# Optimization experiments

Hardware: AMD Instinct MI355X
Metric: run time of the kernel (lower is better)

## Reference

```python
import jax, jax.numpy as jnp
import numpy as np

D_MODEL = 1024
N_EXPERTS = 8
TOP_K = 2


def setup_inputs() -> dict:
    key = jax.random.key(0)
    k1, k2, k3, k4 = jax.random.split(key, 4)
    B, S, D, E = 4, 2048, D_MODEL, N_EXPERTS
    dff = 4 * D
    # xavier-uniform style scale for expert weights
    lim = float(np.sqrt(6.0 / (D + dff)))
    return {
        "x": jax.random.normal(k1, (B, S, D), dtype=jnp.float32),
        "router_w": jax.random.normal(k2, (D, E), dtype=jnp.float32) * (1.0 / np.sqrt(D)),
        "router_b": jnp.zeros((E,), dtype=jnp.float32),
        "expert_up": jax.random.uniform(k3, (E, dff, D), dtype=jnp.float32, minval=-lim, maxval=lim),
        "expert_down": jax.random.uniform(k4, (E, D, dff), dtype=jnp.float32, minval=-lim, maxval=lim),
    }


def reference(x, router_w, router_b, expert_up, expert_down):
    B, S, D = x.shape
    E = expert_up.shape[0]
    x_flat = x.reshape(-1, D)                       # [T, D]
    logits = x_flat @ router_w + router_b           # [T, E]
    probs = jax.nn.softmax(logits, axis=-1)
    top_w, top_idx = jax.lax.top_k(probs, TOP_K)    # [T, K]
    # combine per-token top-k weights into a dense [T, E] combine matrix
    comb = jnp.sum(top_w[..., None] * jax.nn.one_hot(top_idx, E, dtype=x.dtype), axis=1)  # [T, E]
    output = jnp.zeros_like(x_flat)
    for e in range(E):  # fixed small expert count
        h = jax.nn.gelu(x_flat @ expert_up[e].T, approximate=False)   # [T, dff]
        out_e = h @ expert_down[e].T                                  # [T, D]
        output = output + comb[:, e:e + 1] * out_e
    return output.reshape(B, S, D)
```

## Files before the change

kernel.cpp:

```cpp
#include <hip/hip_runtime.h>
#include <hip/hip_bf16.h>
#include <cstdint>

#define T_TOK 8192
#define DM 1024
#define NE 8
#define DFF 4096

#define PERX_UP 576
#define PERX_DN 288
#define GEMM_UP_BLOCKS (8 * PERX_UP)

#define CVTX_BLOCKS 4096
#define CVTW_BLOCKS 16384
#define ROUT_BLOCKS 128

typedef __attribute__((ext_vector_type(8))) short bf16x8;
typedef __attribute__((ext_vector_type(4))) float f32x4;

__device__ __forceinline__ unsigned short f2bf(float f) {
  unsigned int b = __float_as_uint(f);
  b += 0x7FFFu + ((b >> 16) & 1u);
  return (unsigned short)(b >> 16);
}

__device__ __forceinline__ float gelu_exact(float v) {
  return 0.5f * v * (1.0f + erff(v * 0.70710678118654752440f));
}

__device__ __forceinline__ void cvt8(const float* __restrict__ src, unsigned short* __restrict__ dst,
                                     size_t i) {
  const f32x4* p = (const f32x4*)src;
  f32x4 a = p[2 * i];
  f32x4 b = p[2 * i + 1];
  union { bf16x8 v; unsigned short u[8]; } o;
  o.u[0] = f2bf(a.x); o.u[1] = f2bf(a.y); o.u[2] = f2bf(a.z); o.u[3] = f2bf(a.w);
  o.u[4] = f2bf(b.x); o.u[5] = f2bf(b.y); o.u[6] = f2bf(b.z); o.u[7] = f2bf(b.w);
  ((bf16x8*)dst)[i] = o.v;
}

__global__ void cvt_kernel(const float* __restrict__ x, unsigned short* __restrict__ xb) {
  cvt8(x, xb, (size_t)blockIdx.x * blockDim.x + threadIdx.x);
}

__global__ void fused_pre_kernel(const float* __restrict__ x, unsigned short* __restrict__ xb,
                                 const float* __restrict__ up, unsigned short* __restrict__ upb,
                                 const float* __restrict__ rw, const float* __restrict__ rb,
                                 int* __restrict__ counts_pad, int* __restrict__ tlist,
                                 float* __restrict__ wlist) {
  const int bid = blockIdx.x;
  if (bid < CVTX_BLOCKS) {
    cvt8(x, xb, (size_t)bid * 256 + threadIdx.x);
    return;
  }
  if (bid < CVTX_BLOCKS + CVTW_BLOCKS) {
    cvt8(up, upb, (size_t)(bid - CVTX_BLOCKS) * 256 + threadIdx.x);
    return;
  }
  const int rblk = bid - CVTX_BLOCKS - CVTW_BLOCKS;
  __shared__ int hcnt[NE], hbase[NE];
  __shared__ int tE1[64], tE2[64], tR1[64], tR2[64];
  __shared__ float tW1[64], tW2[64];
  if (threadIdx.x < NE) hcnt[threadIdx.x] = 0;
  __syncthreads();
  const int wv = threadIdx.x >> 6, lane = threadIdx.x & 63;
#pragma unroll 1
  for (int it = 0; it < 16; ++it) {
    const int lt = wv * 16 + it;
    const int t = rblk * 64 + lt;
    const float* xr = x + (size_t)t * DM;
    float acc[NE];
#pragma unroll
    for (int e = 0; e < NE; ++e) acc[e] = 0.0f;
#pragma unroll
    for (int i = 0; i < 16; ++i) {
      int d = lane + i * 64;
      float xv = xr[d];
      const float* wr = rw + (size_t)d * NE;
#pragma unroll
      for (int e = 0; e < NE; ++e) acc[e] = fmaf(xv, wr[e], acc[e]);
    }
#pragma unroll
    for (int off = 32; off; off >>= 1) {
#pragma unroll
      for (int e = 0; e < NE; ++e) acc[e] += __shfl_xor(acc[e], off);
    }
    if (lane == 0) {
      float m = -1e30f;
#pragma unroll
      for (int e = 0; e < NE; ++e) { acc[e] += rb[e]; m = fmaxf(m, acc[e]); }
      float p[NE]; float s = 0.0f;
#pragma unroll
      for (int e = 0; e < NE; ++e) { p[e] = expf(acc[e] - m); s += p[e]; }
      int e1 = 0; float p1 = p[0];
#pragma unroll
      for (int e = 1; e < NE; ++e) if (p[e] > p1) { p1 = p[e]; e1 = e; }
      int e2 = -1; float p2 = -1e30f;
#pragma unroll
      for (int e = 0; e < NE; ++e) if (e != e1 && p[e] > p2) { p2 = p[e]; e2 = e; }
      float inv = 1.0f / s;
      int r1 = atomicAdd(&hcnt[e1], 1);
      int r2 = atomicAdd(&hcnt[e2], 1);
      tE1[lt] = e1; tR1[lt] = r1; tW1[lt] = p1 * inv;
      tE2[lt] = e2; tR2[lt] = r2; tW2[lt] = p2 * inv;
    }
  }
  __syncthreads();
  if (threadIdx.x < NE)
    hbase[threadIdx.x] = atomicAdd(&counts_pad[threadIdx.x * 16], hcnt[threadIdx.x]);
  __syncthreads();
  if (threadIdx.x < 64) {
    int lt = threadIdx.x;
    int t = rblk * 64 + lt;
    int e = tE1[lt]; int pos = hbase[e] + tR1[lt];
    tlist[e * T_TOK + pos] = t; wlist[e * T_TOK + pos] = tW1[lt];
    e = tE2[lt]; pos = hbase[e] + tR2[lt];
    tlist[e * T_TOK + pos] = t; wlist[e * T_TOK + pos] = tW2[lt];
  }
}

__global__ void prefix_kernel(const int* __restrict__ counts_pad, int* __restrict__ cntc,
                              int* __restrict__ offs,
                              int* __restrict__ wl_up, int* __restrict__ wl_dn) {
  __shared__ int te[144], tr[144], sn;
  if (threadIdx.x == 0) {
    int s = 0, n = 0;
    for (int e = 0; e < NE; ++e) {
      int c = counts_pad[e * 16];
      cntc[e] = c;
      offs[e] = s; s += c;
      int ntile = (c + 127) / 128;
      for (int r = 0; r < ntile; ++r) { te[n] = e; tr[n] = r; ++n; }
    }
    sn = n;
  }
  __syncthreads();
  const int n = sn;
  for (int idx = threadIdx.x; idx < 8 * PERX_UP; idx += blockDim.x) {
    int k = idx / PERX_UP, i = idx % PERX_UP;
    int g0 = (n * k) / 8, g1 = (n * (k + 1)) / 8, gc = g1 - g0;
    int v = -1;
    if (gc > 0 && i < 32 * gc) {
      int ct = i / gc, g = g0 + i % gc;
      v = (te[g] << 24) | (tr[g] << 16) | ct;
    }
    wl_up[idx] = v;
  }
  for (int idx = threadIdx.x; idx < 8 * PERX_DN; idx += blockDim.x) {
    int k = idx / PERX_DN, i = idx % PERX_DN;
    int g0 = (n * k) / 8, g1 = (n * (k + 1)) / 8, gc = g1 - g0;
    int v = -1;
    if (gc > 0 && i < 16 * gc) {
      int kh = i / (8 * gc);
      int rem = i % (8 * gc);
      int ct = rem / gc, g = g0 + rem % gc;
      v = (te[g] << 24) | (tr[g] << 16) | (kh << 8) | ct;
    }
    wl_dn[idx] = v;
  }
}

#define GL2LDS16(g, l) \
  __builtin_amdgcn_global_load_lds((const __attribute__((address_space(1))) unsigned int*)(g), \
                                   (__attribute__((address_space(3))) unsigned int*)(l), 16, 0, 0)

#define VMCNT4   asm volatile("s_waitcnt vmcnt(4)" ::: "memory")
#define VMCNT0   asm volatile("s_waitcnt vmcnt(0)" ::: "memory")
#define LGKM0    asm volatile("s_waitcnt lgkmcnt(0)" ::: "memory")
#define BARRIER() do { asm volatile("" ::: "memory"); __builtin_amdgcn_s_barrier(); asm volatile("" ::: "memory"); } while (0)

#define STAGE(bi, t) do { \
  const int k_ = (t) * 32; \
  GL2LDS16(asrc0 + k_, smem + (bi) * 4096 + wv * 512); \
  GL2LDS16(asrc1 + k_, smem + (bi) * 4096 + wv * 512 + 2048); \
  GL2LDS16(bsrc0 + k_, smem + 8192 + (bi) * 4096 + wv * 512); \
  GL2LDS16(bsrc1 + k_, smem + 8192 + (bi) * 4096 + wv * 512 + 2048); \
} while (0)

#define COMPUTE(bi) do { \
  const unsigned short* sA_ = smem + (bi) * 4096; \
  const unsigned short* sB_ = smem + 8192 + (bi) * 4096; \
  bf16x8 af_[4], bf_[4]; \
  _Pragma("unroll") \
  for (int m_ = 0; m_ < 4; ++m_) af_[m_] = *(const bf16x8*)(sA_ + (wr + m_ * 16 + lr) * 32 + kx); \
  _Pragma("unroll") \
  for (int n_ = 0; n_ < 4; ++n_) bf_[n_] = *(const bf16x8*)(sB_ + (wc + n_ * 16 + lr) * 32 + kx); \
  _Pragma("unroll") \
  for (int m_ = 0; m_ < 4; ++m_) \
    _Pragma("unroll") \
    for (int n_ = 0; n_ < 4; ++n_) \
      acc[m_][n_] = __builtin_amdgcn_mfma_f32_16x16x32_bf16(af_[m_], bf_[n_], acc[m_][n_], 0, 0, 0); \
} while (0)

#define KLOOP(NT) do { \
  STAGE(0, 0); \
  STAGE(1, 1); \
  for (int t = 0; t < (NT); ++t) { \
    const int b_ = t & 1; \
    if (t + 1 < (NT)) { VMCNT4; } else { VMCNT0; } \
    BARRIER(); \
    COMPUTE(b_); \
    if (t + 2 < (NT)) { \
      LGKM0; \
      BARRIER(); \
      STAGE(b_, t + 2); \
    } \
  } \
} while (0)

__global__ __launch_bounds__(256, 4) void gemm_up_kernel(
    const unsigned short* __restrict__ xb, const unsigned short* __restrict__ wb,
    const int* __restrict__ cntc, const int* __restrict__ offs,
    const int* __restrict__ wl, const int* __restrict__ tlist,
    unsigned short* __restrict__ h,
    const float* __restrict__ dn_f32, unsigned short* __restrict__ dn_bf16) {
  if ((int)blockIdx.x >= GEMM_UP_BLOCKS) {
    cvt8(dn_f32, dn_bf16, (size_t)(blockIdx.x - GEMM_UP_BLOCKS) * 256 + threadIdx.x);
    return;
  }
  const int xcd = blockIdx.x & 7, slot = blockIdx.x >> 3;
  const int item = wl[xcd * PERX_UP + slot];
  if (item < 0) return;
  const int e = (item >> 24) & 7, rt = (item >> 16) & 0xFF, ct = item & 0xFF;
  const int cnt = cntc[e];

  __shared__ unsigned short smem[16384];

  const int tid = threadIdx.x;
  const int wv = tid >> 6, ln = tid & 63;
  const int swz = (tid & 3) ^ ((tid >> 3) & 3);

  const int arow = wv * 16 + (ln >> 2);
  int r0 = rt * 128 + arow;
  int r1 = r0 + 64;
  const int tok0 = tlist[e * T_TOK + (r0 < cnt ? r0 : cnt - 1)];
  const int tok1 = tlist[e * T_TOK + (r1 < cnt ? r1 : cnt - 1)];
  const unsigned short* asrc0 = xb + (size_t)tok0 * DM + swz * 8;
  const unsigned short* asrc1 = xb + (size_t)tok1 * DM + swz * 8;

  const unsigned short* bsrc0 =
      wb + (size_t)e * DFF * DM + (size_t)(ct * 128 + arow) * DM + swz * 8;
  const unsigned short* bsrc1 = bsrc0 + (size_t)64 * DM;

  const int wr = (wv >> 1) * 64, wc = (wv & 1) * 64;
  const int lr = ln & 15;
  const int kx = (((ln >> 4) ^ ((lr >> 1) & 3))) * 8;

  f32x4 acc[4][4] = {};

  KLOOP(DM / 32);

  BARRIER();

  unsigned short* sH = smem;
#pragma unroll
  for (int m = 0; m < 4; ++m) {
    int rloc = wr + m * 16 + (ln >> 4) * 4;
#pragma unroll
    for (int j = 0; j < 4; ++j) {
      int row = rloc + j;
#pragma unroll
      for (int n = 0; n < 4; ++n) {
        int col = wc + n * 16 + lr;
        int sl = ((col >> 3) ^ (row & 7)) * 8 + (col & 7);
        sH[row * 128 + sl] = f2bf(gelu_exact(acc[m][n][j]));
      }
    }
  }
  __syncthreads();
  const size_t hbase = (size_t)offs[e];
#pragma unroll
  for (int it = 0; it < 8; ++it) {
    int idx = it * 256 + tid;
    int row = idx >> 4, c8 = idx & 15;
    if (rt * 128 + row < cnt) {
      unsigned short* hp = h + (hbase + rt * 128 + row) * (size_t)DFF + ct * 128 + c8 * 8;
      *(bf16x8*)hp = *(const bf16x8*)&sH[row * 128 + (c8 ^ (row & 7)) * 8];
    }
  }
}

__global__ __launch_bounds__(256, 4) void gemm_down_kernel(
    const unsigned short* __restrict__ h, const unsigned short* __restrict__ wb,
    const int* __restrict__ cntc, const int* __restrict__ offs,
    const int* __restrict__ wl, const int* __restrict__ tlist,
    const float* __restrict__ wlist, float* __restrict__ out) {
  const int xcd = blockIdx.x & 7, slot = blockIdx.x >> 3;
  const int item = wl[xcd * PERX_DN + slot];
  if (item < 0) return;
  const int e = (item >> 24) & 7, rt = (item >> 16) & 0xFF;
  const int kh = (item >> 8) & 1, ct = item & 0xFF;
  const int cnt = cntc[e];

  __shared__ unsigned short smem[16384];

  const int tid = threadIdx.x;
  const int wv = tid >> 6, ln = tid & 63;
  const int swz = (tid & 3) ^ ((tid >> 3) & 3);
  const size_t hbase = (size_t)offs[e];
  const int kbase = kh * (DFF / 2);

  const int arow = wv * 16 + (ln >> 2);
  int r0 = rt * 128 + arow;
  int r1 = r0 + 64;
  const unsigned short* asrc0 =
      h + (hbase + (r0 < cnt ? r0 : cnt - 1)) * (size_t)DFF + kbase + swz * 8;
  const unsigned short* asrc1 =
      h + (hbase + (r1 < cnt ? r1 : cnt - 1)) * (size_t)DFF + kbase + swz * 8;

  const unsigned short* bsrc0 =
      wb + (size_t)e * DM * DFF + (size_t)(ct * 128 + arow) * DFF + kbase + swz * 8;
  const unsigned short* bsrc1 = bsrc0 + (size_t)64 * DFF;

  const int wr = (wv >> 1) * 64, wc = (wv & 1) * 64;
  const int lr = ln & 15;
  const int kx = (((ln >> 4) ^ ((lr >> 1) & 3))) * 8;

  f32x4 acc[4][4] = {};

  KLOOP(DFF / 2 / 32);

#pragma unroll
  for (int m = 0; m < 4; ++m) {
    int rloc = wr + m * 16 + (ln >> 4) * 4;
#pragma unroll
    for (int j = 0; j < 4; ++j) {
      int row = rt * 128 + rloc + j;
      if (row < cnt) {
        int tok = tlist[e * T_TOK + row];
        float w = wlist[e * T_TOK + row];
        float* op = out + (size_t)tok * DM + ct * 128 + wc + lr;
#pragma unroll
        for (int n = 0; n < 4; ++n) atomicAdd(op + n * 16, w * acc[m][n][j]);
      }
    }
  }
}

extern "C" void kernel_launch(void* const* d_in, const int* in_sizes, int n_in,
                              void* d_out, int out_size, void* d_ws, size_t ws_size,
                              hipStream_t stream) {
  const float* x  = (const float*)d_in[0];
  const float* rw = (const float*)d_in[1];
  const float* rb = (const float*)d_in[2];
  const float* up = (const float*)d_in[3];
  const float* dn = (const float*)d_in[4];
  float* out = (float*)d_out;
  char* ws = (char*)d_ws;

  int*   counts_pad = (int*)(ws + 0);
  int*   cntc   = (int*)(ws + 1024);
  int*   offs   = (int*)(ws + 2048);
  int*   wl_up  = (int*)(ws + 4096);
  int*   wl_dn  = (int*)(ws + 24576);
  int*   tlist  = (int*)(ws + 65536);
  float* wlist  = (float*)(ws + 65536 + 262144);
  unsigned short* xb    = (unsigned short*)(ws + 589824);
  unsigned short* h     = (unsigned short*)(ws + 17367040);
  unsigned short* wbufA = (unsigned short*)(ws + 151584768);
  unsigned short* wbufB = (unsigned short*)(ws + 218693632);
  const bool big_ws = (ws_size >= (size_t)218693632 + 67108864);

  hipMemsetAsync(counts_pad, 0, 512, stream);
  hipMemsetAsync(d_out, 0, (size_t)T_TOK * DM * sizeof(float), stream);

  fused_pre_kernel<<<dim3(CVTX_BLOCKS + CVTW_BLOCKS + ROUT_BLOCKS), 256, 0, stream>>>(
      x, xb, up, wbufA, rw, rb, counts_pad, tlist, wlist);
  prefix_kernel<<<dim3(1), 256, 0, stream>>>(counts_pad, cntc, offs, wl_up, wl_dn);

  if (big_ws) {
    gemm_up_kernel<<<dim3(GEMM_UP_BLOCKS + CVTW_BLOCKS), 256, 0, stream>>>(
        xb, wbufA, cntc, offs, wl_up, tlist, h, dn, wbufB);
    gemm_down_kernel<<<dim3(8 * PERX_DN), 256, 0, stream>>>(
        h, wbufB, cntc, offs, wl_dn, tlist, wlist, out);
  } else {
    gemm_up_kernel<<<dim3(GEMM_UP_BLOCKS), 256, 0, stream>>>(
        xb, wbufA, cntc, offs, wl_up, tlist, h, dn, wbufA);
    cvt_kernel<<<dim3(CVTW_BLOCKS), 256, 0, stream>>>(dn, (unsigned short*)wbufA);
    gemm_down_kernel<<<dim3(8 * PERX_DN), 256, 0, stream>>>(
        h, wbufA, cntc, offs, wl_dn, tlist, wlist, out);
  }
}
```

Baseline: 667.5 us.

## Enlarge expert GEMM tiles to 256x256 with 512-thread blocks

Both expert GEMM kernels move from 128x128 output tiles with 256 threads to 256x256 tiles with 512 threads (8 waves, each computing 128x64). The work lists, tile counts, shared memory layout and the fused weight-conversion tail are all reworked to match. Bigger tiles double the data reuse per staged K-slice and halve global/LDS traffic per FLOP. The cost is double the LDS per block, more accumulator registers, fewer blocks (lower occupancy and worse tail balance across CUs), and more wasted rows at the ragged end of each expert's token count.

Measured after the change: 1.178 ms. 1.77x slower.

```diff
diff --git a/kernel.cpp b/kernel.cpp
--- a/kernel.cpp
+++ b/kernel.cpp
@@ -7,8 +7,8 @@
 #define NE 8
 #define DFF 4096
 
-#define PERX_UP 576
-#define PERX_DN 288
+#define PERX_UP 144
+#define PERX_DN 72
 #define GEMM_UP_BLOCKS (8 * PERX_UP)
 
 #define CVTX_BLOCKS 4096
@@ -122,14 +122,14 @@
 __global__ void prefix_kernel(const int* __restrict__ counts_pad, int* __restrict__ cntc,
                               int* __restrict__ offs,
                               int* __restrict__ wl_up, int* __restrict__ wl_dn) {
-  __shared__ int te[144], tr[144], sn;
+  __shared__ int te[80], tr[80], sn;
   if (threadIdx.x == 0) {
     int s = 0, n = 0;
     for (int e = 0; e < NE; ++e) {
       int c = counts_pad[e * 16];
       cntc[e] = c;
       offs[e] = s; s += c;
-      int ntile = (c + 127) / 128;
+      int ntile = (c + 255) / 256;
       for (int r = 0; r < ntile; ++r) { te[n] = e; tr[n] = r; ++n; }
     }
     sn = n;
@@ -140,7 +140,7 @@
     int k = idx / PERX_UP, i = idx % PERX_UP;
     int g0 = (n * k) / 8, g1 = (n * (k + 1)) / 8, gc = g1 - g0;
     int v = -1;
-    if (gc > 0 && i < 32 * gc) {
+    if (gc > 0 && i < 16 * gc) {
       int ct = i / gc, g = g0 + i % gc;
       v = (te[g] << 24) | (tr[g] << 16) | ct;
     }
@@ -150,9 +150,9 @@
     int k = idx / PERX_DN, i = idx % PERX_DN;
     int g0 = (n * k) / 8, g1 = (n * (k + 1)) / 8, gc = g1 - g0;
     int v = -1;
-    if (gc > 0 && i < 16 * gc) {
-      int kh = i / (8 * gc);
-      int rem = i % (8 * gc);
+    if (gc > 0 && i < 8 * gc) {
+      int kh = i / (4 * gc);
+      int rem = i % (4 * gc);
       int ct = rem / gc, g = g0 + rem % gc;
       v = (te[g] << 24) | (tr[g] << 16) | (kh << 8) | ct;
     }
@@ -171,22 +171,22 @@
 
 #define STAGE(bi, t) do { \
   const int k_ = (t) * 32; \
-  GL2LDS16(asrc0 + k_, smem + (bi) * 4096 + wv * 512); \
-  GL2LDS16(asrc1 + k_, smem + (bi) * 4096 + wv * 512 + 2048); \
-  GL2LDS16(bsrc0 + k_, smem + 8192 + (bi) * 4096 + wv * 512); \
-  GL2LDS16(bsrc1 + k_, smem + 8192 + (bi) * 4096 + wv * 512 + 2048); \
+  GL2LDS16(asrc0 + k_, smem + (bi) * 8192 + tid * 8); \
+  GL2LDS16(asrc1 + k_, smem + (bi) * 8192 + 4096 + tid * 8); \
+  GL2LDS16(bsrc0 + k_, smem + 16384 + (bi) * 8192 + tid * 8); \
+  GL2LDS16(bsrc1 + k_, smem + 16384 + (bi) * 8192 + 4096 + tid * 8); \
 } while (0)
 
 #define COMPUTE(bi) do { \
-  const unsigned short* sA_ = smem + (bi) * 4096; \
-  const unsigned short* sB_ = smem + 8192 + (bi) * 4096; \
-  bf16x8 af_[4], bf_[4]; \
+  const unsigned short* sA_ = smem + (bi) * 8192; \
+  const unsigned short* sB_ = smem + 16384 + (bi) * 8192; \
+  bf16x8 af_[8], bf_[4]; \
   _Pragma("unroll") \
-  for (int m_ = 0; m_ < 4; ++m_) af_[m_] = *(const bf16x8*)(sA_ + (wr + m_ * 16 + lr) * 32 + kx); \
+  for (int m_ = 0; m_ < 8; ++m_) af_[m_] = *(const bf16x8*)(sA_ + (wr + m_ * 16 + lr) * 32 + kx); \
   _Pragma("unroll") \
   for (int n_ = 0; n_ < 4; ++n_) bf_[n_] = *(const bf16x8*)(sB_ + (wc + n_ * 16 + lr) * 32 + kx); \
   _Pragma("unroll") \
-  for (int m_ = 0; m_ < 4; ++m_) \
+  for (int m_ = 0; m_ < 8; ++m_) \
     _Pragma("unroll") \
     for (int n_ = 0; n_ < 4; ++n_) \
       acc[m_][n_] = __builtin_amdgcn_mfma_f32_16x16x32_bf16(af_[m_], bf_[n_], acc[m_][n_], 0, 0, 0); \
@@ -208,14 +208,16 @@
   } \
 } while (0)
 
-__global__ __launch_bounds__(256, 4) void gemm_up_kernel(
+__global__ __launch_bounds__(512, 2) void gemm_up_kernel(
     const unsigned short* __restrict__ xb, const unsigned short* __restrict__ wb,
     const int* __restrict__ cntc, const int* __restrict__ offs,
     const int* __restrict__ wl, const int* __restrict__ tlist,
     unsigned short* __restrict__ h,
     const float* __restrict__ dn_f32, unsigned short* __restrict__ dn_bf16) {
   if ((int)blockIdx.x >= GEMM_UP_BLOCKS) {
-    cvt8(dn_f32, dn_bf16, (size_t)(blockIdx.x - GEMM_UP_BLOCKS) * 256 + threadIdx.x);
+    size_t base = (size_t)(blockIdx.x - GEMM_UP_BLOCKS) * 512 + threadIdx.x;
+    cvt8(dn_f32, dn_bf16, base);
+    cvt8(dn_f32, dn_bf16, base + (size_t)(CVTW_BLOCKS / 4) * 512);
     return;
   }
   const int xcd = blockIdx.x & 7, slot = blockIdx.x >> 3;
@@ -224,63 +226,68 @@
   const int e = (item >> 24) & 7, rt = (item >> 16) & 0xFF, ct = item & 0xFF;
   const int cnt = cntc[e];
 
-  __shared__ unsigned short smem[16384];
+  __shared__ unsigned short smem[32768];
 
   const int tid = threadIdx.x;
-  const int wv = tid >> 6, ln = tid & 63;
+  const int wid = tid >> 6, ln = tid & 63;
   const int swz = (tid & 3) ^ ((tid >> 3) & 3);
 
-  const int arow = wv * 16 + (ln >> 2);
-  int r0 = rt * 128 + arow;
-  int r1 = r0 + 64;
+  int r0 = rt * 256 + (tid >> 2), r1 = r0 + 128;
   const int tok0 = tlist[e * T_TOK + (r0 < cnt ? r0 : cnt - 1)];
   const int tok1 = tlist[e * T_TOK + (r1 < cnt ? r1 : cnt - 1)];
   const unsigned short* asrc0 = xb + (size_t)tok0 * DM + swz * 8;
   const unsigned short* asrc1 = xb + (size_t)tok1 * DM + swz * 8;
 
   const unsigned short* bsrc0 =
-      wb + (size_t)e * DFF * DM + (size_t)(ct * 128 + arow) * DM + swz * 8;
-  const unsigned short* bsrc1 = bsrc0 + (size_t)64 * DM;
-
-  const int wr = (wv >> 1) * 64, wc = (wv & 1) * 64;
-  const int lr = ln & 15;
-  const int kx = (((ln >> 4) ^ ((lr >> 1) & 3))) * 8;
-
-  f32x4 acc[4][4] = {};
+      wb + (size_t)e * DFF * DM + (size_t)(ct * 256 + (tid >> 2)) * DM + swz * 8;
+  const unsigned short* bsrc1 = bsrc0 + (size_t)128 * DM;
+
+  const int wr = (wid >> 2) * 128, wc = (wid & 3) * 64;
+  const int lr = ln & 15, g4 = ln >> 4;
+  const int kx = ((g4 ^ ((lr >> 1) & 3))) * 8;
+
+  f32x4 acc[8][4] = {};
 
   KLOOP(DM / 32);
 
   BARRIER();
 
   unsigned short* sH = smem;
-#pragma unroll
-  for (int m = 0; m < 4; ++m) {
-    int rloc = wr + m * 16 + (ln >> 4) * 4;
-#pragma unroll
-    for (int j = 0; j < 4; ++j) {
-      int row = rloc + j;
-#pragma unroll
-      for (int n = 0; n < 4; ++n) {
-        int col = wc + n * 16 + lr;
-        int sl = ((col >> 3) ^ (row & 7)) * 8 + (col & 7);
-        sH[row * 128 + sl] = f2bf(gelu_exact(acc[m][n][j]));
+  const size_t hbase = (size_t)offs[e];
+#pragma unroll 1
+  for (int half = 0; half < 2; ++half) {
+    if ((wid >> 2) == half) {
+#pragma unroll
+      for (int m = 0; m < 8; ++m) {
+        int rloc = m * 16 + g4 * 4;
+#pragma unroll
+        for (int j = 0; j < 4; ++j) {
+          int row = rloc + j;
+#pragma unroll
+          for (int n = 0; n < 4; ++n) {
+            int col = wc + n * 16 + lr;
+            int sl = ((col >> 3) ^ (row & 7)) * 8 + (col & 7);
+            sH[row * 256 + sl] = f2bf(gelu_exact(acc[m][n][j]));
+          }
+        }
       }
     }
-  }
-  __syncthreads();
-  const size_t hbase = (size_t)offs[e];
-#pragma unroll
-  for (int it = 0; it < 8; ++it) {
-    int idx = it * 256 + tid;
-    int row = idx >> 4, c8 = idx & 15;
-    if (rt * 128 + row < cnt) {
-      unsigned short* hp = h + (hbase + rt * 128 + row) * (size_t)DFF + ct * 128 + c8 * 8;
-      *(bf16x8*)hp = *(const bf16x8*)&sH[row * 128 + (c8 ^ (row & 7)) * 8];
-    }
-  }
-}
-
-__global__ __launch_bounds__(256, 4) void gemm_down_kernel(
+    __syncthreads();
+#pragma unroll
+    for (int it = 0; it < 8; ++it) {
+      int idx = it * 512 + tid;
+      int row = idx >> 5, c8 = idx & 31;
+      int grow = rt * 256 + half * 128 + row;
+      if (grow < cnt) {
+        unsigned short* hp = h + (hbase + grow) * (size_t)DFF + ct * 256 + c8 * 8;
+        *(bf16x8*)hp = *(const bf16x8*)&sH[row * 256 + (c8 ^ (row & 7)) * 8];
+      }
+    }
+    __syncthreads();
+  }
+}
+
+__global__ __launch_bounds__(512, 2) void gemm_down_kernel(
     const unsigned short* __restrict__ h, const unsigned short* __restrict__ wb,
     const int* __restrict__ cntc, const int* __restrict__ offs,
     const int* __restrict__ wl, const int* __restrict__ tlist,
@@ -292,44 +299,42 @@
   const int kh = (item >> 8) & 1, ct = item & 0xFF;
   const int cnt = cntc[e];
 
-  __shared__ unsigned short smem[16384];
+  __shared__ unsigned short smem[32768];
 
   const int tid = threadIdx.x;
-  const int wv = tid >> 6, ln = tid & 63;
+  const int wid = tid >> 6, ln = tid & 63;
   const int swz = (tid & 3) ^ ((tid >> 3) & 3);
   const size_t hbase = (size_t)offs[e];
   const int kbase = kh * (DFF / 2);
 
-  const int arow = wv * 16 + (ln >> 2);
-  int r0 = rt * 128 + arow;
-  int r1 = r0 + 64;
+  int r0 = rt * 256 + (tid >> 2), r1 = r0 + 128;
   const unsigned short* asrc0 =
       h + (hbase + (r0 < cnt ? r0 : cnt - 1)) * (size_t)DFF + kbase + swz * 8;
   const unsigned short* asrc1 =
       h + (hbase + (r1 < cnt ? r1 : cnt - 1)) * (size_t)DFF + kbase + swz * 8;
 
   const unsigned short* bsrc0 =
-      wb + (size_t)e * DM * DFF + (size_t)(ct * 128 + arow) * DFF + kbase + swz * 8;
-  const unsigned short* bsrc1 = bsrc0 + (size_t)64 * DFF;
-
-  const int wr = (wv >> 1) * 64, wc = (wv & 1) * 64;
-  const int lr = ln & 15;
-  const int kx = (((ln >> 4) ^ ((lr >> 1) & 3))) * 8;
-
-  f32x4 acc[4][4] = {};
+      wb + (size_t)e * DM * DFF + (size_t)(ct * 256 + (tid >> 2)) * DFF + kbase + swz * 8;
+  const unsigned short* bsrc1 = bsrc0 + (size_t)128 * DFF;
+
+  const int wr = (wid >> 2) * 128, wc = (wid & 3) * 64;
+  const int lr = ln & 15, g4 = ln >> 4;
+  const int kx = ((g4 ^ ((lr >> 1) & 3))) * 8;
+
+  f32x4 acc[8][4] = {};
 
   KLOOP(DFF / 2 / 32);
 
 #pragma unroll
-  for (int m = 0; m < 4; ++m) {
-    int rloc = wr + m * 16 + (ln >> 4) * 4;
+  for (int m = 0; m < 8; ++m) {
+    int rloc = wr + m * 16 + g4 * 4;
 #pragma unroll
     for (int j = 0; j < 4; ++j) {
-      int row = rt * 128 + rloc + j;
+      int row = rt * 256 + rloc + j;
       if (row < cnt) {
         int tok = tlist[e * T_TOK + row];
         float w = wlist[e * T_TOK + row];
-        float* op = out + (size_t)tok * DM + ct * 128 + wc + lr;
+        float* op = out + (size_t)tok * DM + ct * 256 + wc + lr;
 #pragma unroll
         for (int n = 0; n < 4; ++n) atomicAdd(op + n * 16, w * acc[m][n][j]);
       }
@@ -369,15 +374,15 @@
   prefix_kernel<<<dim3(1), 256, 0, stream>>>(counts_pad, cntc, offs, wl_up, wl_dn);
 
   if (big_ws) {
-    gemm_up_kernel<<<dim3(GEMM_UP_BLOCKS + CVTW_BLOCKS), 256, 0, stream>>>(
+    gemm_up_kernel<<<dim3(GEMM_UP_BLOCKS + CVTW_BLOCKS / 4), 512, 0, stream>>>(
         xb, wbufA, cntc, offs, wl_up, tlist, h, dn, wbufB);
-    gemm_down_kernel<<<dim3(8 * PERX_DN), 256, 0, stream>>>(
+    gemm_down_kernel<<<dim3(8 * PERX_DN), 512, 0, stream>>>(
         h, wbufB, cntc, offs, wl_dn, tlist, wlist, out);
   } else {
-    gemm_up_kernel<<<dim3(GEMM_UP_BLOCKS), 256, 0, stream>>>(
+    gemm_up_kernel<<<dim3(GEMM_UP_BLOCKS), 512, 0, stream>>>(
         xb, wbufA, cntc, offs, wl_up, tlist, h, dn, wbufA);
     cvt_kernel<<<dim3(CVTW_BLOCKS), 256, 0, stream>>>(dn, (unsigned short*)wbufA);
-    gemm_down_kernel<<<dim3(8 * PERX_DN), 256, 0, stream>>>(
+    gemm_down_kernel<<<dim3(8 * PERX_DN), 512, 0, stream>>>(
         h, wbufA, cntc, offs, wl_dn, tlist, wlist, out);
   }
 }
```
